# Performance work log

Measured on AMD Instinct MI355X. Metric: run time of the kernel, lower is better.

## Reference

```python
import jax, jax.numpy as jnp
import numpy as np

N = 100000
E = 1600000
NEG_SLOPE = 0.2


def gat_layer(x, W, al, ar, b, src, dst):
    """DGL GATConv (no dropout, no residual, bias=True, activation=None).
    x: [N, in]; W: [in, H*D]; al, ar, b: [H, D]. Returns [N, H, D]."""
    H, D = al.shape
    feat = (x @ W).reshape(N, H, D)               # [N,H,D]
    el = jnp.sum(feat * al, axis=-1)              # [N,H]
    er = jnp.sum(feat * ar, axis=-1)              # [N,H]
    e = jax.nn.leaky_relu(el[src] + er[dst], NEG_SLOPE)  # [E,H]
    # segment softmax over incoming edges of each dst node
    emax = jax.lax.stop_gradient(jax.ops.segment_max(e, dst, num_segments=N))
    ex = jnp.exp(e - emax[dst])                   # [E,H]
    denom = jax.ops.segment_sum(ex, dst, num_segments=N)  # [N,H]
    alpha = ex / jnp.where(denom[dst] == 0, 1.0, denom[dst])  # [E,H]
    msg = feat[src] * alpha[..., None]            # [E,H,D] gather + weight
    out = jax.ops.segment_sum(msg, dst, num_segments=N)    # [N,H,D] scatter-add
    return out + b[None, :, :]


def setup_inputs() -> dict:
    key = jax.random.key(0)
    ks = jax.random.split(key, 12)
    in_size, hid, out_size, heads = 128, 32, 16, 4
    x = jax.random.normal(ks[0], (N, in_size), dtype=jnp.float32)
    src = jax.random.randint(ks[1], (E,), 0, N, dtype=jnp.int32)
    dst = jax.random.randint(ks[2], (E,), 0, N, dtype=jnp.int32)
    W1 = jax.random.normal(ks[3], (in_size, heads * hid), dtype=jnp.float32) * (1.0 / np.sqrt(in_size))
    al1 = jax.random.normal(ks[4], (heads, hid), dtype=jnp.float32) * 0.1
    ar1 = jax.random.normal(ks[5], (heads, hid), dtype=jnp.float32) * 0.1
    b1 = jnp.zeros((heads, hid), dtype=jnp.float32)
    W2 = jax.random.normal(ks[6], (hid, out_size), dtype=jnp.float32) * (1.0 / np.sqrt(hid))
    al2 = jax.random.normal(ks[7], (1, out_size), dtype=jnp.float32) * 0.1
    ar2 = jax.random.normal(ks[8], (1, out_size), dtype=jnp.float32) * 0.1
    b2 = jnp.zeros((1, out_size), dtype=jnp.float32)
    return {"x": x, "src": src, "dst": dst, "W1": W1, "al1": al1, "ar1": ar1,
            "b1": b1, "W2": W2, "al2": al2, "ar2": ar2, "b2": b2}


def reference(x, src, dst, W1, al1, ar1, b1, W2, al2, ar2, b2):
    h = gat_layer(x, W1, al1, ar1, b1, src, dst)   # [N, heads, hid]
    h = jax.nn.relu(jnp.mean(h, axis=1))           # mean over heads + relu
    h = gat_layer(h, W2, al2, ar2, b2, src, dst)   # [N, 1, out]
    return h.reshape(N, -1)                        # flatten
```

## Files before the change

kernel.cpp:

```cpp
#include <hip/hip_runtime.h>
#include <hip/hip_bf16.h>

#define NEG_SLOPE 0.2f
#define G_SHIFT 7
#define GSZ 128
#define CHUNK 4096

__global__ __launch_bounds__(256) void coarse_scatter(
    const int* __restrict__ src, const int* __restrict__ dst,
    int* __restrict__ gcursor, unsigned* __restrict__ inter, int NB, int E) {
    __shared__ int hist[800];
    __shared__ int lbase[800];
    __shared__ int gbase[800];
    __shared__ unsigned stage[CHUNK];
    __shared__ unsigned short bstage[CHUNK];

    const int tid = threadIdx.x;
    const int e0 = blockIdx.x * CHUNK;
    const int cnt = min(CHUNK, E - e0);

    for (int i = tid; i < NB; i += 256) hist[i] = 0;
    __syncthreads();

    unsigned pk[16];
    int bb[16];
#pragma unroll
    for (int r = 0; r < 16; ++r) {
        int idx = tid + r * 256;
        if (idx < cnt) {
            int s = src[e0 + idx];
            int d = dst[e0 + idx];
            pk[r] = ((unsigned)s << G_SHIFT) | (unsigned)(d & (GSZ - 1));
            bb[r] = d >> G_SHIFT;
            atomicAdd(&hist[bb[r]], 1);
        }
    }
    __syncthreads();
    if (tid < 64) {
        int carry = 0;
        for (int i = 0; i < NB; i += 64) {
            int v = (i + tid < NB) ? hist[i + tid] : 0;
            int xv = v;
            for (int o = 1; o < 64; o <<= 1) {
                int tt = __shfl_up(xv, o, 64);
                if (tid >= o) xv += tt;
            }
            if (i + tid < NB) lbase[i + tid] = carry + xv - v;
            carry += __shfl(xv, 63, 64);
        }
    }
    __syncthreads();
    for (int i = tid; i < NB; i += 256) {
        int hh = hist[i];
        gbase[i] = (hh > 0) ? (i * CHUNK + atomicAdd(&gcursor[i], hh)) : 0;
    }
    __syncthreads();
    for (int i = tid; i < NB; i += 256) hist[i] = 0;
    __syncthreads();
#pragma unroll
    for (int r = 0; r < 16; ++r) {
        int idx = tid + r * 256;
        if (idx < cnt) {
            int b = bb[r];
            int rk = atomicAdd(&hist[b], 1);
            int pos = lbase[b] + rk;
            stage[pos] = pk[r];
            bstage[pos] = (unsigned short)b;
        }
    }
    __syncthreads();
#pragma unroll
    for (int r = 0; r < 16; ++r) {
        int idx = tid + r * 256;
        if (idx < cnt) {
            int b = (int)bstage[idx];
            inter[gbase[b] + (idx - lbase[b])] = stage[idx];
        }
    }
}

__global__ __launch_bounds__(256) void fine_scatter(
    const unsigned* __restrict__ inter, const int* __restrict__ gcursor,
    int* __restrict__ deg, int* __restrict__ rowptr, int* __restrict__ esrc,
    int N, int NB) {
    __shared__ int h[GSZ];
    __shared__ int lb[GSZ];
    __shared__ int stage[CHUNK];
    __shared__ int redsum[256];
    const int b = blockIdx.x;
    const int tid = threadIdx.x;
    const int cnt = gcursor[b];
    const unsigned* ep = inter + (size_t)b * CHUNK;

    {
        int s = 0;
        for (int i = tid; i < b; i += 256) s += gcursor[i];
        redsum[tid] = s;
        __syncthreads();
        for (int o = 128; o > 0; o >>= 1) {
            if (tid < o) redsum[tid] += redsum[tid + o];
            __syncthreads();
        }
    }
    const int base = redsum[0];

    if (tid < GSZ) h[tid] = 0;
    __syncthreads();

    int ss[16];
    unsigned char ln[16];
    int nr = 0;
    for (int idx = tid; idx < cnt; idx += 256) {
        unsigned ed = ep[idx];
        ss[nr] = (int)(ed >> G_SHIFT);
        int l = (int)(ed & (GSZ - 1));
        ln[nr++] = (unsigned char)l;
        atomicAdd(&h[l], 1);
    }
    __syncthreads();
    if (tid < 64) {
        int carry = 0;
        for (int i = 0; i < GSZ; i += 64) {
            int v = h[i + tid];
            int xv = v;
            for (int o = 1; o < 64; o <<= 1) {
                int tt = __shfl_up(xv, o, 64);
                if (tid >= o) xv += tt;
            }
            lb[i + tid] = carry + xv - v;
            carry += __shfl(xv, 63, 64);
        }
    }
    __syncthreads();
    if (tid < GSZ) {
        int node = b * GSZ + tid;
        if (node < N) {
            deg[node] = h[tid];
            rowptr[node] = base + lb[tid];
        }
        h[tid] = 0;
    }
    __syncthreads();
    for (int r = 0; r < nr; ++r) {
        int l = ln[r];
        int rk = atomicAdd(&h[l], 1);
        stage[lb[l] + rk] = ss[r];
    }
    __syncthreads();
    for (int idx = tid; idx < cnt; idx += 256) esrc[base + idx] = stage[idx];
}

__global__ __launch_bounds__(256) void gemm1_fused(
    const float* __restrict__ x, const float* __restrict__ W,
    const float* __restrict__ al, const float* __restrict__ ar,
    __hip_bfloat16* __restrict__ outb, float* __restrict__ el,
    float* __restrict__ er, int N) {
    const int K = 128, C = 128, BK = 32;
    __shared__ float xs[BK][68];
    __shared__ float ws[BK][C];

    const int t = threadIdx.x;
    const int trow = t >> 4;
    const int tcol = t & 15;
    const int m0 = blockIdx.x * 64;

    float acc[4][8];
#pragma unroll
    for (int i = 0; i < 4; ++i)
#pragma unroll
        for (int j = 0; j < 8; ++j) acc[i][j] = 0.f;

    for (int k0 = 0; k0 < K; k0 += BK) {
        {
            const float4* W4 = (const float4*)(W + k0 * C);
#pragma unroll
            for (int r = 0; r < 4; ++r) {
                int q = t + 256 * r;
                int k = q >> 5;
                int c4 = q & 31;
                float4 v = W4[k * 32 + c4];
                *((float4*)&ws[k][c4 * 4]) = v;
            }
        }
        {
#pragma unroll
            for (int r = 0; r < 2; ++r) {
                int q = t + 256 * r;
                int m = q >> 3;
                int k4 = q & 7;
                int gm = m0 + m;
                if (gm >= N) gm = N - 1;
                float4 v = *((const float4*)(x + (size_t)gm * K + k0 + k4 * 4));
                xs[k4 * 4 + 0][m] = v.x;
                xs[k4 * 4 + 1][m] = v.y;
                xs[k4 * 4 + 2][m] = v.z;
                xs[k4 * 4 + 3][m] = v.w;
            }
        }
        __syncthreads();

#pragma unroll
        for (int k = 0; k < BK; ++k) {
            float4 a = *((const float4*)&xs[k][trow * 4]);
            float4 b0 = *((const float4*)&ws[k][tcol * 8]);
            float4 b1 = *((const float4*)&ws[k][tcol * 8 + 4]);
            float av[4] = {a.x, a.y, a.z, a.w};
            float bv[8] = {b0.x, b0.y, b0.z, b0.w, b1.x, b1.y, b1.z, b1.w};
#pragma unroll
            for (int i = 0; i < 4; ++i)
#pragma unroll
                for (int j = 0; j < 8; ++j) acc[i][j] += av[i] * bv[j];
        }
        __syncthreads();
    }

    const int h = tcol >> 2;
    const int d0 = (tcol & 3) * 8;
    float alv[8], arv[8];
#pragma unroll
    for (int j = 0; j < 8; ++j) {
        alv[j] = al[h * 32 + d0 + j];
        arv[j] = ar[h * 32 + d0 + j];
    }
#pragma unroll
    for (int i = 0; i < 4; ++i) {
        int gm = m0 + trow * 4 + i;
        if (gm < N) {
            union { __hip_bfloat16 hh[8]; uint4 u; } pk;
#pragma unroll
            for (int j = 0; j < 8; ++j) pk.hh[j] = __float2bfloat16(acc[i][j]);
            *((uint4*)(outb + (size_t)gm * C + tcol * 8)) = pk.u;
        }
        float pl = 0.f, pr = 0.f;
#pragma unroll
        for (int j = 0; j < 8; ++j) {
            pl += acc[i][j] * alv[j];
            pr += acc[i][j] * arv[j];
        }
        pl += __shfl_xor(pl, 1); pl += __shfl_xor(pl, 2);
        pr += __shfl_xor(pr, 1); pr += __shfl_xor(pr, 2);
        if ((tcol & 3) == 0 && gm < N) {
            el[gm * 4 + h] = pl;
            er[gm * 4 + h] = pr;
        }
    }
}

__device__ __forceinline__ float bf2f(unsigned short v) {
    return __uint_as_float((unsigned)v << 16);
}

__global__ __launch_bounds__(256) void pull1_kernel(
    const int* __restrict__ rowptr, const int* __restrict__ deg,
    const int* __restrict__ esrc, const float* __restrict__ el,
    const float* __restrict__ er, const __hip_bfloat16* __restrict__ featb,
    const float* __restrict__ b,
    const float* __restrict__ W2, const float* __restrict__ al2,
    const float* __restrict__ ar2, float* __restrict__ feat2,
    float* __restrict__ el2, float* __restrict__ er2, int N) {
    int tid = blockIdx.x * 256 + threadIdx.x;
    int node = tid >> 5;
    int lane = threadIdx.x & 31;
    int h = lane >> 3;
    int d4 = lane & 7;
    if (node >= N) return;

    int start = rowptr[node];
    int cnt = deg[node];
    float er_nh = er[node * 4 + h];
    const int* ep = esrc + start;
    const unsigned short* fb = (const unsigned short*)featb + h * 32 + d4 * 4;

    float4 acc = make_float4(0.f, 0.f, 0.f, 0.f);
    float sumex = 0.f;

    int i = 0;
    for (; i + 4 <= cnt; i += 4) {
        int s0 = ep[i], s1 = ep[i + 1], s2 = ep[i + 2], s3 = ep[i + 3];
        float e0 = el[s0 * 4 + h], e1 = el[s1 * 4 + h];
        float e2 = el[s2 * 4 + h], e3 = el[s3 * 4 + h];
        ushort4 u0 = *((const ushort4*)(fb + (size_t)s0 * 128));
        ushort4 u1 = *((const ushort4*)(fb + (size_t)s1 * 128));
        ushort4 u2 = *((const ushort4*)(fb + (size_t)s2 * 128));
        ushort4 u3 = *((const ushort4*)(fb + (size_t)s3 * 128));
        float v0 = e0 + er_nh; v0 = v0 > 0.f ? v0 : NEG_SLOPE * v0;
        float v1 = e1 + er_nh; v1 = v1 > 0.f ? v1 : NEG_SLOPE * v1;
        float v2 = e2 + er_nh; v2 = v2 > 0.f ? v2 : NEG_SLOPE * v2;
        float v3 = e3 + er_nh; v3 = v3 > 0.f ? v3 : NEG_SLOPE * v3;
        float x0 = __expf(v0), x1 = __expf(v1), x2 = __expf(v2), x3 = __expf(v3);
        acc.x += x0 * bf2f(u0.x); acc.y += x0 * bf2f(u0.y);
        acc.z += x0 * bf2f(u0.z); acc.w += x0 * bf2f(u0.w);
        acc.x += x1 * bf2f(u1.x); acc.y += x1 * bf2f(u1.y);
        acc.z += x1 * bf2f(u1.z); acc.w += x1 * bf2f(u1.w);
        acc.x += x2 * bf2f(u2.x); acc.y += x2 * bf2f(u2.y);
        acc.z += x2 * bf2f(u2.z); acc.w += x2 * bf2f(u2.w);
        acc.x += x3 * bf2f(u3.x); acc.y += x3 * bf2f(u3.y);
        acc.z += x3 * bf2f(u3.z); acc.w += x3 * bf2f(u3.w);
        sumex += x0 + x1 + x2 + x3;
    }
    for (; i < cnt; ++i) {
        int s = ep[i];
        float v = el[s * 4 + h] + er_nh;
        v = v > 0.f ? v : NEG_SLOPE * v;
        float ex = __expf(v);
        ushort4 u = *((const ushort4*)(fb + (size_t)s * 128));
        acc.x += ex * bf2f(u.x); acc.y += ex * bf2f(u.y);
        acc.z += ex * bf2f(u.z); acc.w += ex * bf2f(u.w);
        sumex += ex;
    }
    float inv = 1.f / ((sumex == 0.f) ? 1.f : sumex);
    float4 bb = *((const float4*)(b + h * 32 + d4 * 4));
    float4 o;
    o.x = acc.x * inv + bb.x;
    o.y = acc.y * inv + bb.y;
    o.z = acc.z * inv + bb.z;
    o.w = acc.w * inv + bb.w;
    o.x += __shfl_xor(o.x, 8); o.x += __shfl_xor(o.x, 16);
    o.y += __shfl_xor(o.y, 8); o.y += __shfl_xor(o.y, 16);
    o.z += __shfl_xor(o.z, 8); o.z += __shfl_xor(o.z, 16);
    o.w += __shfl_xor(o.w, 8); o.w += __shfl_xor(o.w, 16);
    float4 hb;
    hb.x = fmaxf(o.x * 0.25f, 0.f);
    hb.y = fmaxf(o.y * 0.25f, 0.f);
    hb.z = fmaxf(o.z * 0.25f, 0.f);
    hb.w = fmaxf(o.w * 0.25f, 0.f);

    int c = lane & 15;
    const float* w2c = W2 + c;
    float fc = 0.f;
#pragma unroll
    for (int j = 0; j < 8; ++j) {
        float4 hbj;
        hbj.x = __shfl(hb.x, j, 32);
        hbj.y = __shfl(hb.y, j, 32);
        hbj.z = __shfl(hb.z, j, 32);
        hbj.w = __shfl(hb.w, j, 32);
        fc += hbj.x * w2c[(j * 4 + 0) * 16];
        fc += hbj.y * w2c[(j * 4 + 1) * 16];
        fc += hbj.z * w2c[(j * 4 + 2) * 16];
        fc += hbj.w * w2c[(j * 4 + 3) * 16];
    }
    float pl = fc * al2[c];
    float pr = fc * ar2[c];
    pl += __shfl_xor(pl, 1, 32); pl += __shfl_xor(pl, 2, 32);
    pl += __shfl_xor(pl, 4, 32); pl += __shfl_xor(pl, 8, 32);
    pr += __shfl_xor(pr, 1, 32); pr += __shfl_xor(pr, 2, 32);
    pr += __shfl_xor(pr, 4, 32); pr += __shfl_xor(pr, 8, 32);
    if (lane < 16) feat2[(size_t)node * 16 + c] = fc;
    if (lane == 0) {
        el2[node] = pl;
        er2[node] = pr;
    }
}

__global__ __launch_bounds__(256) void pull2_kernel(
    const int* __restrict__ rowptr, const int* __restrict__ deg,
    const int* __restrict__ esrc, const float* __restrict__ el,
    const float* __restrict__ er, const float* __restrict__ feat,
    const float* __restrict__ b, float* __restrict__ outp, int N) {
    int tid = blockIdx.x * 256 + threadIdx.x;
    int node = tid >> 2;
    int d4 = threadIdx.x & 3;
    if (node >= N) return;

    int start = rowptr[node];
    int cnt = deg[node];
    float er_n = er[node];
    const int* ep = esrc + start;
    const float* fb = feat + d4 * 4;

    float4 acc = make_float4(0.f, 0.f, 0.f, 0.f);
    float sumex = 0.f;
    int i = 0;
    for (; i + 8 <= cnt; i += 8) {
        int s[8];
#pragma unroll
        for (int j = 0; j < 8; ++j) s[j] = ep[i + j];
        float ee[8];
        float4 ff[8];
#pragma unroll
        for (int j = 0; j < 8; ++j) {
            ee[j] = el[s[j]];
            ff[j] = *((const float4*)(fb + (size_t)s[j] * 16));
        }
#pragma unroll
        for (int j = 0; j < 8; ++j) {
            float v = ee[j] + er_n;
            v = v > 0.f ? v : NEG_SLOPE * v;
            float ex = __expf(v);
            acc.x += ex * ff[j].x; acc.y += ex * ff[j].y;
            acc.z += ex * ff[j].z; acc.w += ex * ff[j].w;
            sumex += ex;
        }
    }
    for (; i + 4 <= cnt; i += 4) {
        int s[4];
#pragma unroll
        for (int j = 0; j < 4; ++j) s[j] = ep[i + j];
        float ee[4];
        float4 ff[4];
#pragma unroll
        for (int j = 0; j < 4; ++j) {
            ee[j] = el[s[j]];
            ff[j] = *((const float4*)(fb + (size_t)s[j] * 16));
        }
#pragma unroll
        for (int j = 0; j < 4; ++j) {
            float v = ee[j] + er_n;
            v = v > 0.f ? v : NEG_SLOPE * v;
            float ex = __expf(v);
            acc.x += ex * ff[j].x; acc.y += ex * ff[j].y;
            acc.z += ex * ff[j].z; acc.w += ex * ff[j].w;
            sumex += ex;
        }
    }
    for (; i < cnt; ++i) {
        int s = ep[i];
        float v = el[s] + er_n;
        v = v > 0.f ? v : NEG_SLOPE * v;
        float ex = __expf(v);
        float4 f = *((const float4*)(fb + (size_t)s * 16));
        acc.x += ex * f.x; acc.y += ex * f.y;
        acc.z += ex * f.z; acc.w += ex * f.w;
        sumex += ex;
    }
    float inv = 1.f / ((sumex == 0.f) ? 1.f : sumex);
    float4 bb = *((const float4*)(b + d4 * 4));
    float4 o;
    o.x = acc.x * inv + bb.x;
    o.y = acc.y * inv + bb.y;
    o.z = acc.z * inv + bb.z;
    o.w = acc.w * inv + bb.w;
    *((float4*)(outp + (size_t)node * 16 + d4 * 4)) = o;
}

extern "C" void kernel_launch(void* const* d_in, const int* in_sizes, int n_in,
                              void* d_out, int out_size, void* d_ws, size_t ws_size,
                              hipStream_t stream) {
    const float* x   = (const float*)d_in[0];
    const int*   src = (const int*)d_in[1];
    const int*   dst = (const int*)d_in[2];
    const float* W1  = (const float*)d_in[3];
    const float* al1 = (const float*)d_in[4];
    const float* ar1 = (const float*)d_in[5];
    const float* b1  = (const float*)d_in[6];
    const float* W2  = (const float*)d_in[7];
    const float* al2 = (const float*)d_in[8];
    const float* ar2 = (const float*)d_in[9];
    const float* b2  = (const float*)d_in[10];

    const int E = in_sizes[1];
    const int N = in_sizes[0] / 128;
    const int H1 = 4, C1 = 128;
    const int D2 = 16;
    const int NB = (N + GSZ - 1) / GSZ;
    const int NCH = (E + CHUNK - 1) / CHUNK;

    char* p = (char*)d_ws;
    auto alloc_f = [&](size_t n) { float* q = (float*)p; p += n * sizeof(float); return q; };
    auto alloc_i = [&](size_t n) { int* q = (int*)p; p += n * sizeof(int); return q; };

    __hip_bfloat16* feat1b = (__hip_bfloat16*)p; p += (size_t)N * C1 * sizeof(__hip_bfloat16);
    float* el1   = alloc_f((size_t)N * H1);
    float* er1   = alloc_f((size_t)N * H1);
    float* feat2 = alloc_f((size_t)N * D2);
    float* el2   = alloc_f(N);
    float* er2   = alloc_f(N);
    int* deg     = alloc_i(N);
    int* rowptr  = alloc_i(N);
    int* esrc    = alloc_i(E);
    int* gcursor = alloc_i(NB);
    unsigned* inter = (unsigned*)alloc_i((size_t)NB * CHUNK);

    const int TB = 256;
    auto blocks = [&](long long n) { return (int)((n + TB - 1) / TB); };

    hipMemsetAsync(gcursor, 0, (size_t)NB * sizeof(int), stream);
    coarse_scatter<<<NCH, TB, 0, stream>>>(src, dst, gcursor, inter, NB, E);
    fine_scatter<<<NB, TB, 0, stream>>>(inter, gcursor, deg, rowptr, esrc, N, NB);

    gemm1_fused<<<(N + 63) / 64, TB, 0, stream>>>(x, W1, al1, ar1, feat1b, el1, er1, N);
    pull1_kernel<<<blocks((long long)N * 32), TB, 0, stream>>>(
        rowptr, deg, esrc, el1, er1, feat1b, b1,
        W2, al2, ar2, feat2, el2, er2, N);

    pull2_kernel<<<blocks((long long)N * 4), TB, 0, stream>>>(
        rowptr, deg, esrc, el2, er2, feat2, b2, (float*)d_out, N);
}
```

Measured before the change: 292.7 us.

## Use bf16 MFMA for layer-1 GEMM and widen pull1 gathers to 16 lanes

Replaces the FP32 SIMT GEMM for the first projection with a bf16 MFMA kernel. The kernel converts x to bf16 in shared memory, uses a pre-transposed bf16 copy of W1 made by a small new kernel, and computes el/er from the rounded bf16 outputs. pull1 now maps each node to 16 lanes with 16-byte feature gathers and an 8-edge unrolled loop, which halves the thread count and raises memory-level parallelism per lane. Rounding x to bf16 adds some numerical error, and each thread now holds more registers.

```diff
diff --git a/kernel.cpp b/kernel.cpp
--- a/kernel.cpp
+++ b/kernel.cpp
@@ -5,6 +5,17 @@
 #define G_SHIFT 7
 #define GSZ 128
 #define CHUNK 4096
+
+typedef __attribute__((ext_vector_type(8))) __bf16 bf16x8;
+typedef __attribute__((ext_vector_type(4))) float f32x4;
+
+__device__ __forceinline__ unsigned short f2bf(float f) {
+    unsigned u = __float_as_uint(f);
+    unsigned r = (u + 0x7fffu + ((u >> 16) & 1u)) >> 16;
+    return (unsigned short)r;
+}
+__device__ __forceinline__ float bflo(unsigned v) { return __uint_as_float(v << 16); }
+__device__ __forceinline__ float bfhi(unsigned v) { return __uint_as_float(v & 0xffff0000u); }
 
 __global__ __launch_bounds__(256) void coarse_scatter(
     const int* __restrict__ src, const int* __restrict__ dst,
@@ -150,203 +161,226 @@
     for (int idx = tid; idx < cnt; idx += 256) esrc[base + idx] = stage[idx];
 }
 
-__global__ __launch_bounds__(256) void gemm1_fused(
-    const float* __restrict__ x, const float* __restrict__ W,
+__global__ __launch_bounds__(256) void wconv_kernel(
+    const float* __restrict__ W, unsigned short* __restrict__ wtb) {
+    int t = threadIdx.x;
+    for (int idx = t; idx < 128 * 128; idx += 256) {
+        int c = idx >> 7, k = idx & 127;
+        wtb[idx] = f2bf(W[k * 128 + c]);
+    }
+}
+
+#define GSTRIDE 136
+__global__ __launch_bounds__(256) void gemm1_mfma(
+    const float* __restrict__ x, const unsigned short* __restrict__ wtb,
     const float* __restrict__ al, const float* __restrict__ ar,
-    __hip_bfloat16* __restrict__ outb, float* __restrict__ el,
+    unsigned short* __restrict__ featb, float* __restrict__ el,
     float* __restrict__ er, int N) {
-    const int K = 128, C = 128, BK = 32;
-    __shared__ float xs[BK][68];
-    __shared__ float ws[BK][C];
-
+    __shared__ unsigned short xs[128][GSTRIDE];
+    __shared__ unsigned short ws[128][GSTRIDE];
     const int t = threadIdx.x;
-    const int trow = t >> 4;
-    const int tcol = t & 15;
-    const int m0 = blockIdx.x * 64;
-
-    float acc[4][8];
-#pragma unroll
-    for (int i = 0; i < 4; ++i)
-#pragma unroll
-        for (int j = 0; j < 8; ++j) acc[i][j] = 0.f;
-
-    for (int k0 = 0; k0 < K; k0 += BK) {
-        {
-            const float4* W4 = (const float4*)(W + k0 * C);
-#pragma unroll
-            for (int r = 0; r < 4; ++r) {
-                int q = t + 256 * r;
-                int k = q >> 5;
-                int c4 = q & 31;
-                float4 v = W4[k * 32 + c4];
-                *((float4*)&ws[k][c4 * 4]) = v;
+    const int m0 = blockIdx.x * 128;
+    const int w = t >> 6;
+    const int l = t & 63;
+    const int lr = l & 15;
+    const int lg = l >> 4;
+
+    {
+        const uint4* wv = (const uint4*)wtb;
+#pragma unroll
+        for (int rr = 0; rr < 8; ++rr) {
+            int q = t + 256 * rr;
+            int c = q >> 4, kb = q & 15;
+            uint4 v = wv[q];
+            *((uint4*)&ws[c][kb * 8]) = v;
+        }
+    }
+    {
+#pragma unroll
+        for (int rr = 0; rr < 16; ++rr) {
+            int q = t + 256 * rr;
+            int row = q >> 5, c4 = q & 31;
+            int gm = m0 + row;
+            if (gm >= N) gm = N - 1;
+            float4 v = *((const float4*)(x + (size_t)gm * 128 + c4 * 4));
+            ushort4 o;
+            o.x = f2bf(v.x); o.y = f2bf(v.y); o.z = f2bf(v.z); o.w = f2bf(v.w);
+            *((ushort4*)&xs[row][c4 * 4]) = o;
+        }
+    }
+    __syncthreads();
+
+    f32x4 acc[2][8];
+#pragma unroll
+    for (int i = 0; i < 2; ++i)
+#pragma unroll
+        for (int j = 0; j < 8; ++j) acc[i][j] = (f32x4){0.f, 0.f, 0.f, 0.f};
+
+#pragma unroll
+    for (int kk = 0; kk < 4; ++kk) {
+        const int k0 = kk * 32 + lg * 8;
+        bf16x8 a0 = *((const bf16x8*)&xs[w * 32 + lr][k0]);
+        bf16x8 a1 = *((const bf16x8*)&xs[w * 32 + 16 + lr][k0]);
+#pragma unroll
+        for (int nj = 0; nj < 8; ++nj) {
+            bf16x8 bfr = *((const bf16x8*)&ws[nj * 16 + lr][k0]);
+            acc[0][nj] = __builtin_amdgcn_mfma_f32_16x16x32_bf16(a0, bfr, acc[0][nj], 0, 0, 0);
+            acc[1][nj] = __builtin_amdgcn_mfma_f32_16x16x32_bf16(a1, bfr, acc[1][nj], 0, 0, 0);
+        }
+    }
+    __syncthreads();
+#pragma unroll
+    for (int mi = 0; mi < 2; ++mi)
+#pragma unroll
+        for (int r = 0; r < 4; ++r) {
+            int row = w * 32 + mi * 16 + lg * 4 + r;
+#pragma unroll
+            for (int nj = 0; nj < 8; ++nj)
+                xs[row][nj * 16 + lr] = f2bf(acc[mi][nj][r]);
+        }
+    __syncthreads();
+    {
+        int row = t >> 1, half = t & 1;
+        int gm = m0 + row;
+        if (gm < N) {
+            float pl0 = 0.f, pl1 = 0.f, pr0 = 0.f, pr1 = 0.f;
+            const unsigned short* xr = &xs[row][half * 64];
+            uint4* outp = (uint4*)(featb + (size_t)gm * 128 + half * 64);
+#pragma unroll
+            for (int b8 = 0; b8 < 8; ++b8) {
+                uint4 v = *((const uint4*)(xr + b8 * 8));
+                int cb = half * 64 + b8 * 8;
+                float4 a0 = *((const float4*)(al + cb));
+                float4 a1 = *((const float4*)(al + cb + 4));
+                float4 r0 = *((const float4*)(ar + cb));
+                float4 r1 = *((const float4*)(ar + cb + 4));
+                float f0 = bflo(v.x), f1 = bfhi(v.x), f2 = bflo(v.y), f3 = bfhi(v.y);
+                float f4 = bflo(v.z), f5 = bfhi(v.z), f6 = bflo(v.w), f7 = bfhi(v.w);
+                float sl = f0 * a0.x + f1 * a0.y + f2 * a0.z + f3 * a0.w
+                         + f4 * a1.x + f5 * a1.y + f6 * a1.z + f7 * a1.w;
+                float sr = f0 * r0.x + f1 * r0.y + f2 * r0.z + f3 * r0.w
+                         + f4 * r1.x + f5 * r1.y + f6 * r1.z + f7 * r1.w;
+                if (b8 < 4) { pl0 += sl; pr0 += sr; } else { pl1 += sl; pr1 += sr; }
+                outp[b8] = v;
             }
-        }
-        {
-#pragma unroll
-            for (int r = 0; r < 2; ++r) {
-                int q = t + 256 * r;
-                int m = q >> 3;
-                int k4 = q & 7;
-                int gm = m0 + m;
-                if (gm >= N) gm = N - 1;
-                float4 v = *((const float4*)(x + (size_t)gm * K + k0 + k4 * 4));
-                xs[k4 * 4 + 0][m] = v.x;
-                xs[k4 * 4 + 1][m] = v.y;
-                xs[k4 * 4 + 2][m] = v.z;
-                xs[k4 * 4 + 3][m] = v.w;
-            }
-        }
-        __syncthreads();
-
-#pragma unroll
-        for (int k = 0; k < BK; ++k) {
-            float4 a = *((const float4*)&xs[k][trow * 4]);
-            float4 b0 = *((const float4*)&ws[k][tcol * 8]);
-            float4 b1 = *((const float4*)&ws[k][tcol * 8 + 4]);
-            float av[4] = {a.x, a.y, a.z, a.w};
-            float bv[8] = {b0.x, b0.y, b0.z, b0.w, b1.x, b1.y, b1.z, b1.w};
-#pragma unroll
-            for (int i = 0; i < 4; ++i)
-#pragma unroll
-                for (int j = 0; j < 8; ++j) acc[i][j] += av[i] * bv[j];
-        }
-        __syncthreads();
-    }
-
-    const int h = tcol >> 2;
-    const int d0 = (tcol & 3) * 8;
-    float alv[8], arv[8];
-#pragma unroll
-    for (int j = 0; j < 8; ++j) {
-        alv[j] = al[h * 32 + d0 + j];
-        arv[j] = ar[h * 32 + d0 + j];
-    }
-#pragma unroll
-    for (int i = 0; i < 4; ++i) {
-        int gm = m0 + trow * 4 + i;
-        if (gm < N) {
-            union { __hip_bfloat16 hh[8]; uint4 u; } pk;
-#pragma unroll
-            for (int j = 0; j < 8; ++j) pk.hh[j] = __float2bfloat16(acc[i][j]);
-            *((uint4*)(outb + (size_t)gm * C + tcol * 8)) = pk.u;
-        }
-        float pl = 0.f, pr = 0.f;
-#pragma unroll
-        for (int j = 0; j < 8; ++j) {
-            pl += acc[i][j] * alv[j];
-            pr += acc[i][j] * arv[j];
-        }
-        pl += __shfl_xor(pl, 1); pl += __shfl_xor(pl, 2);
-        pr += __shfl_xor(pr, 1); pr += __shfl_xor(pr, 2);
-        if ((tcol & 3) == 0 && gm < N) {
-            el[gm * 4 + h] = pl;
-            er[gm * 4 + h] = pr;
-        }
-    }
-}
-
-__device__ __forceinline__ float bf2f(unsigned short v) {
-    return __uint_as_float((unsigned)v << 16);
+            el[gm * 4 + half * 2 + 0] = pl0;
+            el[gm * 4 + half * 2 + 1] = pl1;
+            er[gm * 4 + half * 2 + 0] = pr0;
+            er[gm * 4 + half * 2 + 1] = pr1;
+        }
+    }
 }
 
 __global__ __launch_bounds__(256) void pull1_kernel(
     const int* __restrict__ rowptr, const int* __restrict__ deg,
     const int* __restrict__ esrc, const float* __restrict__ el,
-    const float* __restrict__ er, const __hip_bfloat16* __restrict__ featb,
+    const float* __restrict__ er, const unsigned short* __restrict__ featb,
     const float* __restrict__ b,
     const float* __restrict__ W2, const float* __restrict__ al2,
     const float* __restrict__ ar2, float* __restrict__ feat2,
     float* __restrict__ el2, float* __restrict__ er2, int N) {
     int tid = blockIdx.x * 256 + threadIdx.x;
-    int node = tid >> 5;
-    int lane = threadIdx.x & 31;
-    int h = lane >> 3;
-    int d4 = lane & 7;
+    int node = tid >> 4;
+    int lane = threadIdx.x & 15;
     if (node >= N) return;
-
+    int h = lane >> 2;
+    int dq = lane & 3;
     int start = rowptr[node];
     int cnt = deg[node];
     float er_nh = er[node * 4 + h];
     const int* ep = esrc + start;
-    const unsigned short* fb = (const unsigned short*)featb + h * 32 + d4 * 4;
-
-    float4 acc = make_float4(0.f, 0.f, 0.f, 0.f);
+    const unsigned short* fb = featb + h * 32 + dq * 8;
+
+    float acc[8];
+#pragma unroll
+    for (int j = 0; j < 8; ++j) acc[j] = 0.f;
     float sumex = 0.f;
 
     int i = 0;
+    for (; i + 8 <= cnt; i += 8) {
+        int s[8]; float e[8]; uint4 u[8];
+#pragma unroll
+        for (int j = 0; j < 8; ++j) s[j] = ep[i + j];
+#pragma unroll
+        for (int j = 0; j < 8; ++j) u[j] = *((const uint4*)(fb + (size_t)s[j] * 128));
+#pragma unroll
+        for (int j = 0; j < 8; ++j) e[j] = el[s[j] * 4 + h];
+#pragma unroll
+        for (int j = 0; j < 8; ++j) {
+            float v = e[j] + er_nh;
+            v = v > 0.f ? v : NEG_SLOPE * v;
+            float xx = __expf(v);
+            sumex += xx;
+            acc[0] += xx * bflo(u[j].x); acc[1] += xx * bfhi(u[j].x);
+            acc[2] += xx * bflo(u[j].y); acc[3] += xx * bfhi(u[j].y);
+            acc[4] += xx * bflo(u[j].z); acc[5] += xx * bfhi(u[j].z);
+            acc[6] += xx * bflo(u[j].w); acc[7] += xx * bfhi(u[j].w);
+        }
+    }
     for (; i + 4 <= cnt; i += 4) {
-        int s0 = ep[i], s1 = ep[i + 1], s2 = ep[i + 2], s3 = ep[i + 3];
-        float e0 = el[s0 * 4 + h], e1 = el[s1 * 4 + h];
-        float e2 = el[s2 * 4 + h], e3 = el[s3 * 4 + h];
-        ushort4 u0 = *((const ushort4*)(fb + (size_t)s0 * 128));
-        ushort4 u1 = *((const ushort4*)(fb + (size_t)s1 * 128));
-        ushort4 u2 = *((const ushort4*)(fb + (size_t)s2 * 128));
-        ushort4 u3 = *((const ushort4*)(fb + (size_t)s3 * 128));
-        float v0 = e0 + er_nh; v0 = v0 > 0.f ? v0 : NEG_SLOPE * v0;
-        float v1 = e1 + er_nh; v1 = v1 > 0.f ? v1 : NEG_SLOPE * v1;
-        float v2 = e2 + er_nh; v2 = v2 > 0.f ? v2 : NEG_SLOPE * v2;
-        float v3 = e3 + er_nh; v3 = v3 > 0.f ? v3 : NEG_SLOPE * v3;
-        float x0 = __expf(v0), x1 = __expf(v1), x2 = __expf(v2), x3 = __expf(v3);
-        acc.x += x0 * bf2f(u0.x); acc.y += x0 * bf2f(u0.y);
-        acc.z += x0 * bf2f(u0.z); acc.w += x0 * bf2f(u0.w);
-        acc.x += x1 * bf2f(u1.x); acc.y += x1 * bf2f(u1.y);
-        acc.z += x1 * bf2f(u1.z); acc.w += x1 * bf2f(u1.w);
-        acc.x += x2 * bf2f(u2.x); acc.y += x2 * bf2f(u2.y);
-        acc.z += x2 * bf2f(u2.z); acc.w += x2 * bf2f(u2.w);
-        acc.x += x3 * bf2f(u3.x); acc.y += x3 * bf2f(u3.y);
-        acc.z += x3 * bf2f(u3.z); acc.w += x3 * bf2f(u3.w);
-        sumex += x0 + x1 + x2 + x3;
+        int s[4]; float e[4]; uint4 u[4];
+#pragma unroll
+        for (int j = 0; j < 4; ++j) s[j] = ep[i + j];
+#pragma unroll
+        for (int j = 0; j < 4; ++j) u[j] = *((const uint4*)(fb + (size_t)s[j] * 128));
+#pragma unroll
+        for (int j = 0; j < 4; ++j) e[j] = el[s[j] * 4 + h];
+#pragma unroll
+        for (int j = 0; j < 4; ++j) {
+            float v = e[j] + er_nh;
+            v = v > 0.f ? v : NEG_SLOPE * v;
+            float xx = __expf(v);
+            sumex += xx;
+            acc[0] += xx * bflo(u[j].x); acc[1] += xx * bfhi(u[j].x);
+            acc[2] += xx * bflo(u[j].y); acc[3] += xx * bfhi(u[j].y);
+            acc[4] += xx * bflo(u[j].z); acc[5] += xx * bfhi(u[j].z);
+            acc[6] += xx * bflo(u[j].w); acc[7] += xx * bfhi(u[j].w);
+        }
     }
     for (; i < cnt; ++i) {
         int s = ep[i];
         float v = el[s * 4 + h] + er_nh;
         v = v > 0.f ? v : NEG_SLOPE * v;
-        float ex = __expf(v);
-        ushort4 u = *((const ushort4*)(fb + (size_t)s * 128));
-        acc.x += ex * bf2f(u.x); acc.y += ex * bf2f(u.y);
-        acc.z += ex * bf2f(u.z); acc.w += ex * bf2f(u.w);
-        sumex += ex;
-    }
+        float xx = __expf(v);
+        sumex += xx;
+        uint4 u = *((const uint4*)(fb + (size_t)s * 128));
+        acc[0] += xx * bflo(u.x); acc[1] += xx * bfhi(u.x);
+        acc[2] += xx * bflo(u.y); acc[3] += xx * bfhi(u.y);
+        acc[4] += xx * bflo(u.z); acc[5] += xx * bfhi(u.z);
+        acc[6] += xx * bflo(u.w); acc[7] += xx * bfhi(u.w);
+    }
+
     float inv = 1.f / ((sumex == 0.f) ? 1.f : sumex);
-    float4 bb = *((const float4*)(b + h * 32 + d4 * 4));
-    float4 o;
-    o.x = acc.x * inv + bb.x;
-    o.y = acc.y * inv + bb.y;
-    o.z = acc.z * inv + bb.z;
-    o.w = acc.w * inv + bb.w;
-    o.x += __shfl_xor(o.x, 8); o.x += __shfl_xor(o.x, 16);
-    o.y += __shfl_xor(o.y, 8); o.y += __shfl_xor(o.y, 16);
-    o.z += __shfl_xor(o.z, 8); o.z += __shfl_xor(o.z, 16);
-    o.w += __shfl_xor(o.w, 8); o.w += __shfl_xor(o.w, 16);
-    float4 hb;
-    hb.x = fmaxf(o.x * 0.25f, 0.f);
-    hb.y = fmaxf(o.y * 0.25f, 0.f);
-    hb.z = fmaxf(o.z * 0.25f, 0.f);
-    hb.w = fmaxf(o.w * 0.25f, 0.f);
-
-    int c = lane & 15;
-    const float* w2c = W2 + c;
+    float4 bb0 = *((const float4*)(b + h * 32 + dq * 8));
+    float4 bb1 = *((const float4*)(b + h * 32 + dq * 8 + 4));
+    float o[8];
+    o[0] = acc[0] * inv + bb0.x; o[1] = acc[1] * inv + bb0.y;
+    o[2] = acc[2] * inv + bb0.z; o[3] = acc[3] * inv + bb0.w;
+    o[4] = acc[4] * inv + bb1.x; o[5] = acc[5] * inv + bb1.y;
+    o[6] = acc[6] * inv + bb1.z; o[7] = acc[7] * inv + bb1.w;
+#pragma unroll
+    for (int j = 0; j < 8; ++j) {
+        o[j] += __shfl_xor(o[j], 4);
+        o[j] += __shfl_xor(o[j], 8);
+        o[j] = fmaxf(o[j] * 0.25f, 0.f);
+    }
+    int c = lane;
     float fc = 0.f;
 #pragma unroll
-    for (int j = 0; j < 8; ++j) {
-        float4 hbj;
-        hbj.x = __shfl(hb.x, j, 32);
-        hbj.y = __shfl(hb.y, j, 32);
-        hbj.z = __shfl(hb.z, j, 32);
-        hbj.w = __shfl(hb.w, j, 32);
-        fc += hbj.x * w2c[(j * 4 + 0) * 16];
-        fc += hbj.y * w2c[(j * 4 + 1) * 16];
-        fc += hbj.z * w2c[(j * 4 + 2) * 16];
-        fc += hbj.w * w2c[(j * 4 + 3) * 16];
+    for (int q = 0; q < 4; ++q) {
+#pragma unroll
+        for (int j = 0; j < 8; ++j) {
+            float hv = __shfl(o[j], q, 16);
+            fc += hv * W2[(q * 8 + j) * 16 + c];
+        }
     }
     float pl = fc * al2[c];
     float pr = fc * ar2[c];
-    pl += __shfl_xor(pl, 1, 32); pl += __shfl_xor(pl, 2, 32);
-    pl += __shfl_xor(pl, 4, 32); pl += __shfl_xor(pl, 8, 32);
-    pr += __shfl_xor(pr, 1, 32); pr += __shfl_xor(pr, 2, 32);
-    pr += __shfl_xor(pr, 4, 32); pr += __shfl_xor(pr, 8, 32);
-    if (lane < 16) feat2[(size_t)node * 16 + c] = fc;
+    pl += __shfl_xor(pl, 1); pl += __shfl_xor(pl, 2);
+    pl += __shfl_xor(pl, 4); pl += __shfl_xor(pl, 8);
+    pr += __shfl_xor(pr, 1); pr += __shfl_xor(pr, 2);
+    pr += __shfl_xor(pr, 4); pr += __shfl_xor(pr, 8);
+    feat2[(size_t)node * 16 + c] = fc;
     if (lane == 0) {
         el2[node] = pl;
         er2[node] = pr;
@@ -460,7 +494,7 @@
     auto alloc_f = [&](size_t n) { float* q = (float*)p; p += n * sizeof(float); return q; };
     auto alloc_i = [&](size_t n) { int* q = (int*)p; p += n * sizeof(int); return q; };
 
-    __hip_bfloat16* feat1b = (__hip_bfloat16*)p; p += (size_t)N * C1 * sizeof(__hip_bfloat16);
+    unsigned short* feat1b = (unsigned short*)p; p += (size_t)N * C1 * sizeof(unsigned short);
     float* el1   = alloc_f((size_t)N * H1);
     float* er1   = alloc_f((size_t)N * H1);
     float* feat2 = alloc_f((size_t)N * D2);
@@ -471,16 +505,18 @@
     int* esrc    = alloc_i(E);
     int* gcursor = alloc_i(NB);
     unsigned* inter = (unsigned*)alloc_i((size_t)NB * CHUNK);
+    unsigned short* wtb = (unsigned short*)p; p += (size_t)128 * 128 * sizeof(unsigned short);
 
     const int TB = 256;
     auto blocks = [&](long long n) { return (int)((n + TB - 1) / TB); };
 
     hipMemsetAsync(gcursor, 0, (size_t)NB * sizeof(int), stream);
+    wconv_kernel<<<1, TB, 0, stream>>>(W1, wtb);
     coarse_scatter<<<NCH, TB, 0, stream>>>(src, dst, gcursor, inter, NB, E);
     fine_scatter<<<NB, TB, 0, stream>>>(inter, gcursor, deg, rowptr, esrc, N, NB);
 
-    gemm1_fused<<<(N + 63) / 64, TB, 0, stream>>>(x, W1, al1, ar1, feat1b, el1, er1, N);
-    pull1_kernel<<<blocks((long long)N * 32), TB, 0, stream>>>(
+    gemm1_mfma<<<(N + 127) / 128, TB, 0, stream>>>(x, wtb, al1, ar1, feat1b, el1, er1, N);
+    pull1_kernel<<<blocks((long long)N * 16), TB, 0, stream>>>(
         rowptr, deg, esrc, el1, er1, feat1b, b1,
         W2, al2, ar2, feat2, el2, er2, N);
 
```

After: 272.5 us. 1.07x faster.
